# Optimization experiments

Measured on AMD Instinct MI355X. Metric: run time of the kernel, lower is better.

Reference implementation:

```python
import jax, jax.numpy as jnp
import numpy as np

B, N, C, H, W = 32, 64, 3, 512, 512
P = 16               # patch_size
NUM_CLASSES = 128


def setup_inputs() -> dict:
    key = jax.random.key(0)
    k1, k2, k3, k4 = jax.random.split(key, 4)
    image = jax.random.normal(k1, (B, C, H, W), dtype=jnp.float32)
    emb = jax.random.normal(k2, (NUM_CLASSES, P * P * 3), dtype=jnp.float32)
    labels = jax.random.randint(k3, (B, N), 0, NUM_CLASSES)
    # precomputed top-left corners; original clamps so corners lie in [0, H-P]
    top_left = jax.random.randint(k4, (B, N, 2), 0, H - P + 1)
    return {"image": image, "emb": emb, "labels": labels, "top_left": top_left}


def reference(image, emb, labels, top_left):
    # gather patches: [B, N, 3, P, P]
    patches = emb[labels].reshape(B, N, 3, P, P)
    # reorder so channel dim trails the advanced-index result dims: [B, N, P, P, 3]
    vals = jnp.transpose(patches, (0, 1, 3, 4, 2))
    bb = jnp.arange(B)[:, None, None, None]                                 # [B,1,1,1]
    rr = top_left[..., 0][:, :, None, None] + jnp.arange(P)[None, None, :, None]  # [B,N,P,1]
    cc = top_left[..., 1][:, :, None, None] + jnp.arange(P)[None, None, None, :]  # [B,N,1,P]
    # scatter-add each patch into the image at its computed offset (overlaps sum)
    return image.at[bb, :, rr, cc].add(vals)
```

## Files before the change

kernel.cpp:

```cpp
#include <hip/hip_runtime.h>
#include <hip/hip_bf16.h>

#define BB   32
#define NN   64
#define CC   3
#define HH   512
#define WW   512
#define PP   16
#define PLANE (HH * WW)

__global__ __launch_bounds__(256)
void ImagePatch_scatter_kernel(const float* __restrict__ emb,
                               const int*   __restrict__ labels,
                               const int*   __restrict__ top_left,
                               float*       __restrict__ out) {
    int t  = blockIdx.x * blockDim.x + threadIdx.x;
    int j  = t & (PP - 1);
    int i  = (t >> 4) & (PP - 1);
    int pn = t >> 8;

    int label = labels[pn];
    int r = top_left[pn * 2 + 0] + i;
    int c = top_left[pn * 2 + 1] + j;
    int b = pn >> 6;

    const float* e = emb + (size_t)label * (CC * PP * PP) + i * PP + j;
    float* o = out + (size_t)b * (CC * PLANE) + (size_t)r * WW + c;

    atomicAdd(o,             e[0]);
    atomicAdd(o + PLANE,     e[PP * PP]);
    atomicAdd(o + 2 * PLANE, e[2 * PP * PP]);
}

extern "C" void kernel_launch(void* const* d_in, const int* in_sizes, int n_in,
                              void* d_out, int out_size, void* d_ws, size_t ws_size,
                              hipStream_t stream) {
    const float* image    = (const float*)d_in[0];
    const float* emb      = (const float*)d_in[1];
    const int*   labels   = (const int*)d_in[2];
    const int*   top_left = (const int*)d_in[3];
    float*       out      = (float*)d_out;

    size_t bytes = (size_t)BB * CC * HH * WW * sizeof(float);
    hipMemcpyAsync(out, image, bytes, hipMemcpyDeviceToDevice, stream);

    int total  = BB * NN * PP * PP;
    int block  = 256;
    int grid   = total / block;
    ImagePatch_scatter_kernel<<<grid, block, 0, stream>>>(emb, labels, top_left, out);
}
```

Baseline: 44.32 us.

## Fuse image copy and patch scatter into a per-row gather kernel

Replaces the device-to-device copy plus atomic scatter with one kernel where each block owns a single image row of a batch element. The block first collects, via a wave ballot, the patches whose rows cover that image row, then each thread loads float4 pixels across three channels, adds any overlapping patch values, and writes the result once. This removes the second pass over the output, the separate copy, and all atomics, at the cost of a per-row patch scan and some divergent inner loops.

```diff
diff --git a/kernel.cpp b/kernel.cpp
--- a/kernel.cpp
+++ b/kernel.cpp
@@ -1,35 +1,74 @@
 #include <hip/hip_runtime.h>
 #include <hip/hip_bf16.h>
 
-#define BB   32
-#define NN   64
-#define CC   3
-#define HH   512
-#define WW   512
-#define PP   16
-#define PLANE (HH * WW)
+#define B_   32
+#define N_   64
+#define C_   3
+#define H_   512
+#define W_   512
+#define P_   16
+#define PLANE (H_ * W_)
+#define IMG   (C_ * PLANE)
 
-__global__ __launch_bounds__(256)
-void ImagePatch_scatter_kernel(const float* __restrict__ emb,
-                               const int*   __restrict__ labels,
-                               const int*   __restrict__ top_left,
-                               float*       __restrict__ out) {
-    int t  = blockIdx.x * blockDim.x + threadIdx.x;
-    int j  = t & (PP - 1);
-    int i  = (t >> 4) & (PP - 1);
-    int pn = t >> 8;
+__global__ __launch_bounds__(128)
+void ImagePatch_fused_kernel(const float* __restrict__ image,
+                             const float* __restrict__ emb,
+                             const int*   __restrict__ labels,
+                             const int*   __restrict__ top_left,
+                             float*       __restrict__ out) {
+    __shared__ int s_cnt;
+    __shared__ int s_dr[N_];
+    __shared__ int s_tc[N_];
+    __shared__ int s_lb[N_];
 
-    int label = labels[pn];
-    int r = top_left[pn * 2 + 0] + i;
-    int c = top_left[pn * 2 + 1] + j;
-    int b = pn >> 6;
+    const int bid = blockIdx.x;
+    const int r   = bid & (H_ - 1);
+    const int b   = bid >> 9;
+    const int tid = threadIdx.x;
 
-    const float* e = emb + (size_t)label * (CC * PP * PP) + i * PP + j;
-    float* o = out + (size_t)b * (CC * PLANE) + (size_t)r * WW + c;
+    if (tid < 64) {
+        const int idx = b * N_ + tid;
+        const int tr  = top_left[idx * 2];
+        const unsigned dr = (unsigned)(r - tr);
+        const bool cover  = dr < P_;
+        const unsigned long long m = __ballot(cover);
+        if (cover) {
+            const int pos = __popcll(m & ((1ull << tid) - 1ull));
+            s_dr[pos] = (int)dr;
+            s_tc[pos] = top_left[idx * 2 + 1];
+            s_lb[pos] = labels[idx];
+        }
+        if (tid == 0) s_cnt = __popcll(m);
+    }
+    __syncthreads();
 
-    atomicAdd(o,             e[0]);
-    atomicAdd(o + PLANE,     e[PP * PP]);
-    atomicAdd(o + 2 * PLANE, e[2 * PP * PP]);
+    const int c0 = tid * 4;
+    const size_t base = (size_t)b * IMG + (size_t)r * W_ + c0;
+
+    float4 v0 = *(const float4*)(image + base);
+    float4 v1 = *(const float4*)(image + base + PLANE);
+    float4 v2 = *(const float4*)(image + base + 2 * PLANE);
+
+    const int cnt = s_cnt;
+    for (int k = 0; k < cnt; ++k) {
+        const int tc = s_tc[k];
+        if (c0 + 3 >= tc && c0 < tc + P_) {
+            const float* e = emb + s_lb[k] * (C_ * P_ * P_) + s_dr[k] * P_;
+            #pragma unroll
+            for (int q = 0; q < 4; ++q) {
+                const unsigned dc = (unsigned)(c0 + q - tc);
+                if (dc < P_) {
+                    ((float*)&v0)[q] += e[dc];
+                    ((float*)&v1)[q] += e[P_ * P_ + dc];
+                    ((float*)&v2)[q] += e[2 * P_ * P_ + dc];
+                }
+            }
+        }
+    }
+
+    *(float4*)(out + base)             = v0;
+    *(float4*)(out + base + PLANE)     = v1;
+    *(float4*)(out + base + 2 * PLANE) = v2;
 }
 
 extern "C" void kernel_launch(void* const* d_in, const int* in_sizes, int n_in,
@@ -41,11 +80,6 @@
     const int*   top_left = (const int*)d_in[3];
     float*       out      = (float*)d_out;
 
-    size_t bytes = (size_t)BB * CC * HH * WW * sizeof(float);
-    hipMemcpyAsync(out, image, bytes, hipMemcpyDeviceToDevice, stream);
-
-    int total  = BB * NN * PP * PP;
-    int block  = 256;
-    int grid   = total / block;
-    ImagePatch_scatter_kernel<<<grid, block, 0, stream>>>(emb, labels, top_left, out);
+    const int grid = B_ * H_;
+    ImagePatch_fused_kernel<<<grid, 128, 0, stream>>>(image, emb, labels, top_left, out);
 }
```

New measurement: 36.53 us. 17.6% less time.
